# Kernel tuning notes

Measured on AMD Instinct MI355X. Metric: run time of the kernel, lower is better.

## Reference

```python
import jax, jax.numpy as jnp
import numpy as np

N = 50000      # num_nodes
E = 800000     # num_edges
D = 128        # hidden_dim
V = 32000      # vocab_size
T = 8          # num_edge_types
NT = 16        # num_node_types


def setup_inputs() -> dict:
    key = jax.random.key(0)
    ks = jax.random.split(key, 10)
    s = 1.0 / np.sqrt(D)
    return {
        "x": jax.random.randint(ks[0], (N,), 0, V),
        "edge_index": jax.random.randint(ks[1], (2, E), 0, N),
        "edge_type": jax.random.randint(ks[2], (E,), 0, T),
        "node_type": jax.random.randint(ks[3], (N,), 0, NT),
        "emb": jax.random.normal(ks[4], (V, D), dtype=jnp.float32) * s,
        "W_rel": jax.random.normal(ks[5], (T, D, D), dtype=jnp.float32) * s,
        "b_node": jax.random.normal(ks[6], (NT, D), dtype=jnp.float32) * 0.01,
        "W_ih": jax.random.normal(ks[7], (3 * D, D), dtype=jnp.float32) * s,
        "W_hh": jax.random.normal(ks[8], (3 * D, D), dtype=jnp.float32) * s,
        "b_ih": jnp.zeros((3 * D,), dtype=jnp.float32),
        "b_hh": jnp.zeros((3 * D,), dtype=jnp.float32),
    }


def _gru_cell(inp, h, W_ih, W_hh, b_ih, b_hh):
    # torch.nn.GRUCell semantics
    gi = inp @ W_ih.T + b_ih   # [N, 3D]
    gh = h @ W_hh.T + b_hh     # [N, 3D]
    i_r, i_z, i_n = jnp.split(gi, 3, axis=-1)
    h_r, h_z, h_n = jnp.split(gh, 3, axis=-1)
    r = jax.nn.sigmoid(i_r + h_r)
    z = jax.nn.sigmoid(i_z + h_z)
    n = jnp.tanh(i_n + r * h_n)
    return (1.0 - z) * n + z * h


def reference(x, edge_index, edge_type, node_type, emb, W_rel, b_node, W_ih, W_hh, b_ih, b_hh):
    h = emb[x]                                   # [N, D] node embeddings
    src, dst = edge_index[0], edge_index[1]
    n_nodes = h.shape[0]
    for _ in range(5):
        # relational message passing: per-edge-type linear on source nodes
        Ht = jnp.einsum('nd,tdf->ntf', h, W_rel)  # [N, T, D] all-type transforms
        msg = Ht[src, edge_type]                  # [E, D] gather per edge
        aggr = jax.ops.segment_sum(msg, dst, num_segments=n_nodes)  # scatter-add to dst
        aggr = aggr + b_node[node_type]           # node-type-specific bias
        h = _gru_cell(aggr, h, W_ih, W_hh, b_ih, b_hh)
    return h
```

## Files before the change

### kernel.cpp

```cpp
#include <hip/hip_runtime.h>
#include <hip/hip_fp16.h>
#include <math.h>

#define N_NODES 50000
#define N_EDGES 800000
#define D 128
#define T_TYPES 8
#define TPAD 136
#define NBLK_SCAN 196
#define TILES 1563

typedef short short8 __attribute__((ext_vector_type(8)));
typedef float float4v __attribute__((ext_vector_type(4)));
typedef unsigned short ushort_t;

static __device__ __forceinline__ unsigned short f2bf(float f) {
    unsigned u = __float_as_uint(f);
    u += 0x7fff + ((u >> 16) & 1);
    return (unsigned short)(u >> 16);
}
static __device__ __forceinline__ float bf2f(unsigned short b) {
    return __uint_as_float((unsigned)b << 16);
}
static __device__ __forceinline__ void splitbf(float x, unsigned short& hi, unsigned short& lo) {
    unsigned short h_ = f2bf(x);
    hi = h_;
    lo = f2bf(x - bf2f(h_));
}

#define GLOAD16(gp, lp) __builtin_amdgcn_global_load_lds( \
    (const __attribute__((address_space(1))) unsigned int*)(gp), \
    (__attribute__((address_space(3))) unsigned int*)(lp), 16, 0, 0)

__global__ void embed_gather(const int* __restrict__ x, const float* __restrict__ emb,
                             ushort_t* __restrict__ hhi, ushort_t* __restrict__ hlo) {
    int n = blockIdx.x;
    int d = threadIdx.x;
    float v = emb[(size_t)x[n] * D + d];
    unsigned short a, b;
    splitbf(v, a, b);
    hhi[(size_t)n * D + d] = a;
    hlo[(size_t)n * D + d] = b;
}

__global__ void convert_wrelT(const float* __restrict__ Wrel,
                              ushort_t* __restrict__ hi, ushort_t* __restrict__ lo) {
    int idx = blockIdx.x * 256 + threadIdx.x;
    int t = idx >> 14;
    int rem = idx & 16383;
    int f = rem >> 7;
    int d = rem & 127;
    unsigned short a, b;
    splitbf(Wrel[((size_t)t << 14) + (d << 7) + f], a, b);
    hi[idx] = a;
    lo[idx] = b;
}

__global__ void convert_w(const float* __restrict__ in,
                          ushort_t* __restrict__ hi, ushort_t* __restrict__ lo, int n) {
    int idx = blockIdx.x * 256 + threadIdx.x;
    if (idx < n) {
        unsigned short a, b;
        splitbf(in[idx], a, b);
        hi[idx] = a;
        lo[idx] = b;
    }
}

__global__ void count_deg(const int* __restrict__ ei, int* __restrict__ deg) {
    int e = blockIdx.x * 256 + threadIdx.x;
    if (e >= N_EDGES) return;
    atomicAdd(&deg[ei[N_EDGES + e]], 1);
}

__global__ __launch_bounds__(256) void scan_blocks(const int* __restrict__ deg,
                                                   int* __restrict__ bsums) {
    __shared__ int red[4];
    int idx = blockIdx.x * 256 + threadIdx.x;
    int v = (idx < N_NODES) ? deg[idx] : 0;
#pragma unroll
    for (int o = 32; o > 0; o >>= 1) v += __shfl_down(v, o);
    if ((threadIdx.x & 63) == 0) red[threadIdx.x >> 6] = v;
    __syncthreads();
    if (threadIdx.x == 0) bsums[blockIdx.x] = red[0] + red[1] + red[2] + red[3];
}

__global__ __launch_bounds__(256) void scan_tops(int* __restrict__ bsums) {
    __shared__ int s[256];
    int tid = threadIdx.x;
    int v = (tid < NBLK_SCAN) ? bsums[tid] : 0;
    s[tid] = v;
    __syncthreads();
#pragma unroll
    for (int o = 1; o < 256; o <<= 1) {
        int u = (tid >= o) ? s[tid - o] : 0;
        __syncthreads();
        s[tid] += u;
        __syncthreads();
    }
    if (tid < NBLK_SCAN) bsums[tid] = s[tid] - v;
}

__global__ __launch_bounds__(256) void scan_final(const int* __restrict__ bsums,
                                                  int* __restrict__ deg_cursor,
                                                  int* __restrict__ rs) {
    __shared__ int s[256];
    int tid = threadIdx.x;
    int idx = blockIdx.x * 256 + tid;
    int v = (idx < N_NODES) ? deg_cursor[idx] : 0;
    s[tid] = v;
    __syncthreads();
#pragma unroll
    for (int o = 1; o < 256; o <<= 1) {
        int u = (tid >= o) ? s[tid - o] : 0;
        __syncthreads();
        s[tid] += u;
        __syncthreads();
    }
    int excl = s[tid] - v + bsums[blockIdx.x];
    if (idx < N_NODES) {
        rs[idx] = excl;
        deg_cursor[idx] = excl;
    }
    if (idx == 0) rs[N_NODES] = N_EDGES;
}

__global__ void fill_csr(const int* __restrict__ ei, const int* __restrict__ et,
                         int* __restrict__ cursor, int* __restrict__ packed) {
    int e = blockIdx.x * 256 + threadIdx.x;
    if (e >= N_EDGES) return;
    int dst = ei[N_EDGES + e];
    int pos = atomicAdd(&cursor[dst], 1);
    packed[pos] = (ei[e] << 3) | et[e];
}

__global__ __launch_bounds__(256, 2) void gemm_rel(const ushort_t* __restrict__ hhi,
                                                   const ushort_t* __restrict__ hlo,
                                                   const ushort_t* __restrict__ Whi,
                                                   const ushort_t* __restrict__ Wlo,
                                                   ushort_t* __restrict__ Ht) {
    __shared__ __align__(16) ushort_t wlds[2][128 * TPAD];
    const int tid = threadIdx.x;
    const int wave = tid >> 6, lane = tid & 63;
    const int q = lane >> 4, li = lane & 15;
    const int t = blockIdx.y;
    const int m_base = blockIdx.x * 128 + wave * 32;

    {
        const ushort_t* gh = Whi + ((size_t)t << 14);
        const ushort_t* gl = Wlo + ((size_t)t << 14);
#pragma unroll
        for (int i = 0; i < 8; ++i) {
            int g = (i * 256 + tid) * 8;
            int row = g >> 7, col = g & 127;
            *(short8*)(&wlds[0][row * TPAD + col]) = *(const short8*)(gh + g);
            *(short8*)(&wlds[1][row * TPAD + col]) = *(const short8*)(gl + g);
        }
    }
    __syncthreads();

    int r0 = m_base + li;      if (r0 > N_NODES - 1) r0 = N_NODES - 1;
    int r1 = m_base + 16 + li; if (r1 > N_NODES - 1) r1 = N_NODES - 1;
    const ushort_t* A0h = hhi + (size_t)r0 * D + q * 8;
    const ushort_t* A0l = hlo + (size_t)r0 * D + q * 8;
    const ushort_t* A1h = hhi + (size_t)r1 * D + q * 8;
    const ushort_t* A1l = hlo + (size_t)r1 * D + q * 8;

    short8 a0h[4], a0l[4], a1h[4], a1l[4];
#pragma unroll
    for (int ks = 0; ks < 4; ++ks) {
        a0h[ks] = *(const short8*)(A0h + ks * 32);
        a0l[ks] = *(const short8*)(A0l + ks * 32);
        a1h[ks] = *(const short8*)(A1h + ks * 32);
        a1l[ks] = *(const short8*)(A1l + ks * 32);
    }

    float4v acc[2][8];
#pragma unroll
    for (int m = 0; m < 2; ++m)
#pragma unroll
        for (int ft = 0; ft < 8; ++ft) acc[m][ft] = (float4v){0.f, 0.f, 0.f, 0.f};

#pragma unroll
    for (int ks = 0; ks < 4; ++ks) {
#pragma unroll
        for (int ft = 0; ft < 8; ++ft) {
            const int lo_off = (ft * 16 + li) * TPAD + ks * 32 + q * 8;
            short8 bh = *(const short8*)(&wlds[0][lo_off]);
            short8 bl = *(const short8*)(&wlds[1][lo_off]);
            acc[0][ft] = __builtin_amdgcn_mfma_f32_16x16x32_bf16(a0h[ks], bh, acc[0][ft], 0, 0, 0);
            acc[0][ft] = __builtin_amdgcn_mfma_f32_16x16x32_bf16(a0l[ks], bh, acc[0][ft], 0, 0, 0);
            acc[0][ft] = __builtin_amdgcn_mfma_f32_16x16x32_bf16(a0h[ks], bl, acc[0][ft], 0, 0, 0);
            acc[1][ft] = __builtin_amdgcn_mfma_f32_16x16x32_bf16(a1h[ks], bh, acc[1][ft], 0, 0, 0);
            acc[1][ft] = __builtin_amdgcn_mfma_f32_16x16x32_bf16(a1l[ks], bh, acc[1][ft], 0, 0, 0);
            acc[1][ft] = __builtin_amdgcn_mfma_f32_16x16x32_bf16(a1h[ks], bl, acc[1][ft], 0, 0, 0);
        }
    }

    __syncthreads();
    ushort_t* tw = &wlds[0][0] + wave * 32 * TPAD;
#pragma unroll
    for (int m = 0; m < 2; ++m)
#pragma unroll
        for (int ft = 0; ft < 8; ++ft)
#pragma unroll
            for (int r = 0; r < 4; ++r) {
                __half hv = __float2half_rn(acc[m][ft][r]);
                tw[(m * 16 + q * 4 + r) * TPAD + ft * 16 + li] = __half_as_ushort(hv);
            }
#pragma unroll
    for (int i = 0; i < 8; ++i) {
        int row = i * 4 + q;
        int col = li * 8;
        short8 v = *(const short8*)(tw + row * TPAD + col);
        int orow = m_base + row;
        if (orow < N_NODES)
            *(short8*)(Ht + (size_t)orow * 1024 + (t << 7) + col) = v;
    }
}

__global__ __launch_bounds__(256) void aggregate_csr(const int* __restrict__ rs,
                                                     const int* __restrict__ packed,
                                                     const ushort_t* __restrict__ Ht,
                                                     const int* __restrict__ nt,
                                                     const float* __restrict__ b_node,
                                                     ushort_t* __restrict__ ahi,
                                                     ushort_t* __restrict__ alo) {
    int n = blockIdx.x * 4 + (threadIdx.x >> 6);
    if (n >= N_NODES) return;
    const int lane = threadIdx.x & 63;
    const int beg = rs[n], end = rs[n + 1];
    const __half2* Ht2 = (const __half2*)Ht;

    float2 acc = ((const float2*)(b_node + (size_t)nt[n] * D))[lane];

    int i = beg;
    for (; i + 3 < end; i += 4) {
        int p0 = packed[i], p1 = packed[i + 1], p2 = packed[i + 2], p3 = packed[i + 3];
        float2 f0 = __half22float2(Ht2[(size_t)p0 * 64 + lane]);
        float2 f1 = __half22float2(Ht2[(size_t)p1 * 64 + lane]);
        float2 f2 = __half22float2(Ht2[(size_t)p2 * 64 + lane]);
        float2 f3 = __half22float2(Ht2[(size_t)p3 * 64 + lane]);
        acc.x += (f0.x + f1.x) + (f2.x + f3.x);
        acc.y += (f0.y + f1.y) + (f2.y + f3.y);
    }
    for (; i < end; ++i) {
        int pk = packed[i];
        float2 fv = __half22float2(Ht2[(size_t)pk * 64 + lane]);
        acc.x += fv.x;
        acc.y += fv.y;
    }

    unsigned short h0, l0, h1, l1;
    splitbf(acc.x, h0, l0);
    splitbf(acc.y, h1, l1);
    ((unsigned*)ahi)[(size_t)n * 64 + lane] = (unsigned)h0 | ((unsigned)h1 << 16);
    ((unsigned*)alo)[(size_t)n * 64 + lane] = (unsigned)l0 | ((unsigned)l1 << 16);
}

__global__ __launch_bounds__(256, 1) void gru_persist(
    const ushort_t* __restrict__ ahi, const ushort_t* __restrict__ alo,
    const ushort_t* __restrict__ hhi_in, const ushort_t* __restrict__ hlo_in,
    ushort_t* __restrict__ hhi_out, ushort_t* __restrict__ hlo_out,
    const ushort_t* __restrict__ Wihi, const ushort_t* __restrict__ Wilo,
    const ushort_t* __restrict__ Whhi, const ushort_t* __restrict__ Whlo,
    const float* __restrict__ b_ih, const float* __restrict__ b_hh,
    float* __restrict__ h, int write_h)
{
    __shared__ __align__(16) ushort_t xlds[2 * 4 * 4096];
    __shared__ __align__(16) ushort_t tbuf[2][32 * 72];

    const int tid = threadIdx.x;
    const int wave = tid >> 6, lane = tid & 63;
    const int q = lane >> 4, li = lane & 15;
    const int bid = blockIdx.x;
    const int fhalf = (bid & 15) >> 3;
    const int s = (bid >> 4) * 8 + (bid & 7);
    const int fl = wave * 16 + li;
    const int fg = fhalf * 64 + fl;

    const size_t oR = (size_t)fg * D + q * 8;
    const size_t oZ = (size_t)(D + fg) * D + q * 8;
    const size_t oN = (size_t)(2 * D + fg) * D + q * 8;
    short8 Wr[12][4];
#pragma unroll
    for (int ks = 0; ks < 4; ++ks) {
        const int off = ks * 32;
        Wr[0][ks]  = *(const short8*)(Wihi + oR + off);
        Wr[1][ks]  = *(const short8*)(Wilo + oR + off);
        Wr[2][ks]  = *(const short8*)(Whhi + oR + off);
        Wr[3][ks]  = *(const short8*)(Whlo + oR + off);
        Wr[4][ks]  = *(const short8*)(Wihi + oZ + off);
        Wr[5][ks]  = *(const short8*)(Wilo + oZ + off);
        Wr[6][ks]  = *(const short8*)(Whhi + oZ + off);
        Wr[7][ks]  = *(const short8*)(Whlo + oZ + off);
        Wr[8][ks]  = *(const short8*)(Wihi + oN + off);
        Wr[9][ks]  = *(const short8*)(Wilo + oN + off);
        Wr[10][ks] = *(const short8*)(Whhi + oN + off);
        Wr[11][ks] = *(const short8*)(Whlo + oN + off);
    }
    const float bR  = b_ih[fg] + b_hh[fg];
    const float bZ  = b_ih[D + fg] + b_hh[D + fg];
    const float bIn = b_ih[2 * D + fg];
    const float bHn = b_hh[2 * D + fg];

    const int lrow_base = wave * 4 + (lane >> 4);
    const int cswz = (lane & 15) ^ (lrow_base & 7);

    {
#pragma unroll
        for (int it = 0; it < 2; ++it) {
            int gr = s * 32 + it * 16 + lrow_base;
            if (gr > N_NODES - 1) gr = N_NODES - 1;
            const size_t so = (size_t)gr * D + cswz * 8;
            ushort_t* l0 = &xlds[(it * 16 + wave * 4) * 128];
            GLOAD16(ahi + so,    l0);
            GLOAD16(alo + so,    l0 + 4096);
            GLOAD16(hhi_in + so, l0 + 8192);
            GLOAD16(hlo_in + so, l0 + 12288);
        }
    }
    __syncthreads();

    int cur = 0;
    for (int tile = s; tile < TILES; tile += 256) {
        const int nxt = tile + 256;
        if (nxt < TILES) {
            ushort_t* nb = &xlds[(cur ^ 1) * 16384];
#pragma unroll
            for (int it = 0; it < 2; ++it) {
                int gr = nxt * 32 + it * 16 + lrow_base;
                if (gr > N_NODES - 1) gr = N_NODES - 1;
                const size_t so = (size_t)gr * D + cswz * 8;
                ushort_t* l0 = nb + (it * 16 + wave * 4) * 128;
                GLOAD16(ahi + so,    l0);
                GLOAD16(alo + so,    l0 + 4096);
                GLOAD16(hhi_in + so, l0 + 8192);
                GLOAD16(hlo_in + so, l0 + 12288);
            }
        }

        const ushort_t* xb = &xlds[cur * 16384];
        float4v aR[2], aZ[2], aI[2], aH[2];
#pragma unroll
        for (int m = 0; m < 2; ++m) {
            aR[m] = (float4v){0.f, 0.f, 0.f, 0.f};
            aZ[m] = aR[m]; aI[m] = aR[m]; aH[m] = aR[m];
        }
#pragma unroll
        for (int ks = 0; ks < 4; ++ks) {
#pragma unroll
            for (int m = 0; m < 2; ++m) {
                const int row = m * 16 + li;
                const int inoff = row * 128 + ((ks * 32 + q * 8) ^ ((row & 7) << 3));
                short8 xah = *(const short8*)(xb + inoff);
                short8 xal = *(const short8*)(xb + 4096 + inoff);
                short8 xhh = *(const short8*)(xb + 8192 + inoff);
                short8 xhl = *(const short8*)(xb + 12288 + inoff);
                aR[m] = __builtin_amdgcn_mfma_f32_16x16x32_bf16(xah, Wr[0][ks], aR[m], 0, 0, 0);
                aR[m] = __builtin_amdgcn_mfma_f32_16x16x32_bf16(xal, Wr[0][ks], aR[m], 0, 0, 0);
                aR[m] = __builtin_amdgcn_mfma_f32_16x16x32_bf16(xah, Wr[1][ks], aR[m], 0, 0, 0);
                aR[m] = __builtin_amdgcn_mfma_f32_16x16x32_bf16(xhh, Wr[2][ks], aR[m], 0, 0, 0);
                aR[m] = __builtin_amdgcn_mfma_f32_16x16x32_bf16(xhl, Wr[2][ks], aR[m], 0, 0, 0);
                aR[m] = __builtin_amdgcn_mfma_f32_16x16x32_bf16(xhh, Wr[3][ks], aR[m], 0, 0, 0);
                aZ[m] = __builtin_amdgcn_mfma_f32_16x16x32_bf16(xah, Wr[4][ks], aZ[m], 0, 0, 0);
                aZ[m] = __builtin_amdgcn_mfma_f32_16x16x32_bf16(xal, Wr[4][ks], aZ[m], 0, 0, 0);
                aZ[m] = __builtin_amdgcn_mfma_f32_16x16x32_bf16(xah, Wr[5][ks], aZ[m], 0, 0, 0);
                aZ[m] = __builtin_amdgcn_mfma_f32_16x16x32_bf16(xhh, Wr[6][ks], aZ[m], 0, 0, 0);
                aZ[m] = __builtin_amdgcn_mfma_f32_16x16x32_bf16(xhl, Wr[6][ks], aZ[m], 0, 0, 0);
                aZ[m] = __builtin_amdgcn_mfma_f32_16x16x32_bf16(xhh, Wr[7][ks], aZ[m], 0, 0, 0);
                aI[m] = __builtin_amdgcn_mfma_f32_16x16x32_bf16(xah, Wr[8][ks], aI[m], 0, 0, 0);
                aI[m] = __builtin_amdgcn_mfma_f32_16x16x32_bf16(xal, Wr[8][ks], aI[m], 0, 0, 0);
                aI[m] = __builtin_amdgcn_mfma_f32_16x16x32_bf16(xah, Wr[9][ks], aI[m], 0, 0, 0);
                aH[m] = __builtin_amdgcn_mfma_f32_16x16x32_bf16(xhh, Wr[10][ks], aH[m], 0, 0, 0);
                aH[m] = __builtin_amdgcn_mfma_f32_16x16x32_bf16(xhl, Wr[10][ks], aH[m], 0, 0, 0);
                aH[m] = __builtin_amdgcn_mfma_f32_16x16x32_bf16(xhh, Wr[11][ks], aH[m], 0, 0, 0);
            }
        }

#pragma unroll
        for (int m = 0; m < 2; ++m) {
#pragma unroll
            for (int r = 0; r < 4; ++r) {
                const int row = m * 16 + q * 4 + r;
                const int hoff = row * 128 + (fg ^ ((row & 7) << 3));
                float hold = bf2f(xb[8192 + hoff]) + bf2f(xb[12288 + hoff]);
                float rg = 1.0f / (1.0f + __expf(-(aR[m][r] + bR)));
                float zg = 1.0f / (1.0f + __expf(-(aZ[m][r] + bZ)));
                float narg = aI[m][r] + bIn + rg * (aH[m][r] + bHn);
                float ex = __expf(2.0f * narg);
                float ng = 1.0f - 2.0f / (ex + 1.0f);
                float hn = (1.0f - zg) * ng + zg * hold;
                unsigned short sh, sl;
                splitbf(hn, sh, sl);
                tbuf[0][row * 72 + fl] = sh;
                tbuf[1][row * 72 + fl] = sl;
            }
        }
        __syncthreads();

        {
            const int row = tid >> 3, col = (tid & 7) * 8;
            const int node = tile * 32 + row;
            if (node < N_NODES) {
                short8 vh = *(const short8*)(&tbuf[0][row * 72 + col]);
                short8 vl = *(const short8*)(&tbuf[1][row * 72 + col]);
                const size_t go = (size_t)node * D + fhalf * 64 + col;
                *(short8*)(hhi_out + go) = vh;
                *(short8*)(hlo_out + go) = vl;
                if (write_h) {
                    float4v f0, f1;
#pragma unroll
                    for (int k2 = 0; k2 < 4; ++k2) {
                        f0[k2] = bf2f((unsigned short)vh[k2]) + bf2f((unsigned short)vl[k2]);
                        f1[k2] = bf2f((unsigned short)vh[4 + k2]) + bf2f((unsigned short)vl[4 + k2]);
                    }
                    *(float4v*)(h + go) = f0;
                    *(float4v*)(h + go + 4) = f1;
                }
            }
        }
        __syncthreads();
        cur ^= 1;
    }
}

extern "C" void kernel_launch(void* const* d_in, const int* in_sizes, int n_in,
                              void* d_out, int out_size, void* d_ws, size_t ws_size,
                              hipStream_t stream) {
    const int* x      = (const int*)d_in[0];
    const int* ei     = (const int*)d_in[1];
    const int* et     = (const int*)d_in[2];
    const int* nt     = (const int*)d_in[3];
    const float* emb  = (const float*)d_in[4];
    const float* Wrel = (const float*)d_in[5];
    const float* b_node = (const float*)d_in[6];
    const float* W_ih = (const float*)d_in[7];
    const float* W_hh = (const float*)d_in[8];
    const float* b_ih = (const float*)d_in[9];
    const float* b_hh = (const float*)d_in[10];

    float* h = (float*)d_out;
    float* ws = (float*)d_ws;

    ushort_t* Ht = (ushort_t*)ws;
    ushort_t* us = (ushort_t*)(ws + 25600000);
    ushort_t* ahi  = us;
    ushort_t* alo  = us + 6400000;
    ushort_t* hhi  = us + 12800000;
    ushort_t* hlo  = us + 19200000;
    ushort_t* Whi  = us + 25600000;
    ushort_t* Wlo  = Whi + 131072;
    ushort_t* Wihi = Wlo + 131072;
    ushort_t* Wilo = Wihi + 49152;
    ushort_t* Whhi = Wilo + 49152;
    ushort_t* Whlo = Whhi + 49152;
    int* rs     = (int*)(ws + 38629376);
    int* packed = rs + 50004;
    int* bsums  = packed + 800000;
    ushort_t* hhi2 = (ushort_t*)(ws + 39479808);
    ushort_t* hlo2 = hhi2 + 6400000;
    int* deg    = (int*)ws;

    convert_wrelT<<<512, 256, 0, stream>>>(Wrel, Whi, Wlo);
    convert_w<<<192, 256, 0, stream>>>(W_ih, Wihi, Wilo, 3 * D * D);
    convert_w<<<192, 256, 0, stream>>>(W_hh, Whhi, Whlo, 3 * D * D);
    embed_gather<<<N_NODES, 128, 0, stream>>>(x, emb, hhi, hlo);

    hipMemsetAsync(deg, 0, 50000 * sizeof(int), stream);
    count_deg<<<3125, 256, 0, stream>>>(ei, deg);
    scan_blocks<<<NBLK_SCAN, 256, 0, stream>>>(deg, bsums);
    scan_tops<<<1, 256, 0, stream>>>(bsums);
    scan_final<<<NBLK_SCAN, 256, 0, stream>>>(bsums, deg, rs);
    fill_csr<<<3125, 256, 0, stream>>>(ei, et, deg, packed);

    for (int it = 0; it < 5; ++it) {
        const ushort_t* hi_in = (it & 1) ? hhi2 : hhi;
        const ushort_t* lo_in = (it & 1) ? hlo2 : hlo;
        ushort_t* hi_out = (it & 1) ? hhi : hhi2;
        ushort_t* lo_out = (it & 1) ? hlo : hlo2;
        dim3 g(391, T_TYPES);
        gemm_rel<<<g, 256, 0, stream>>>(hi_in, lo_in, Whi, Wlo, Ht);
        aggregate_csr<<<12500, 256, 0, stream>>>(rs, packed, Ht, nt, b_node, ahi, alo);
        gru_persist<<<512, 256, 0, stream>>>(ahi, alo, hi_in, lo_in, hi_out, lo_out,
                                             Wihi, Wilo, Whhi, Whlo, b_ih, b_hh,
                                             h, it == 4 ? 1 : 0);
    }
}
```

Baseline: 977.5 us.

## Aggregate raw source features per edge type before applying relational weights

Replaces transform-then-gather with gather-then-transform. Edges are bucketed into a CSR keyed by (type, dst). A scatter kernel sums the source features per bucket into an fp16 buffer S of size T×N×D. A single typed GEMM then multiplies each type slice by W_rel and accumulates across types, adding the node-type bias. This removes the large N×T×D Ht write and its random per-edge gather, at the cost of an fp16 intermediate for the summed features and a split-fp16 weight scheme with a scaled low part, which may reduce accuracy.

```diff
diff --git a/kernel.cpp b/kernel.cpp
--- a/kernel.cpp
+++ b/kernel.cpp
@@ -7,10 +7,12 @@
 #define D 128
 #define T_TYPES 8
 #define TPAD 136
-#define NBLK_SCAN 196
+#define N2 400000
+#define NBLK2 1563
 #define TILES 1563
 
 typedef short short8 __attribute__((ext_vector_type(8)));
+typedef _Float16 half8v __attribute__((ext_vector_type(8)));
 typedef float float4v __attribute__((ext_vector_type(4)));
 typedef unsigned short ushort_t;
 
@@ -43,17 +45,19 @@
     hlo[(size_t)n * D + d] = b;
 }
 
-__global__ void convert_wrelT(const float* __restrict__ Wrel,
-                              ushort_t* __restrict__ hi, ushort_t* __restrict__ lo) {
+__global__ void convert_wrelT_f16(const float* __restrict__ Wrel,
+                                  ushort_t* __restrict__ hi, ushort_t* __restrict__ lo) {
     int idx = blockIdx.x * 256 + threadIdx.x;
     int t = idx >> 14;
     int rem = idx & 16383;
     int f = rem >> 7;
     int d = rem & 127;
-    unsigned short a, b;
-    splitbf(Wrel[((size_t)t << 14) + (d << 7) + f], a, b);
-    hi[idx] = a;
-    lo[idx] = b;
+    float w = Wrel[((size_t)t << 14) + (d << 7) + f];
+    __half wh = __float2half_rn(w);
+    float r = w - __half2float(wh);
+    __half wl = __float2half_rn(r * 2048.0f);
+    hi[idx] = __half_as_ushort(wh);
+    lo[idx] = __half_as_ushort(wl);
 }
 
 __global__ void convert_w(const float* __restrict__ in,
@@ -67,17 +71,18 @@
     }
 }
 
-__global__ void count_deg(const int* __restrict__ ei, int* __restrict__ deg) {
+__global__ void count_deg2(const int* __restrict__ ei, const int* __restrict__ et,
+                           int* __restrict__ deg2) {
     int e = blockIdx.x * 256 + threadIdx.x;
     if (e >= N_EDGES) return;
-    atomicAdd(&deg[ei[N_EDGES + e]], 1);
-}
-
-__global__ __launch_bounds__(256) void scan_blocks(const int* __restrict__ deg,
-                                                   int* __restrict__ bsums) {
+    atomicAdd(&deg2[et[e] * N_NODES + ei[N_EDGES + e]], 1);
+}
+
+__global__ __launch_bounds__(256) void scan_blocks2(const int* __restrict__ deg,
+                                                    int* __restrict__ bsums) {
     __shared__ int red[4];
     int idx = blockIdx.x * 256 + threadIdx.x;
-    int v = (idx < N_NODES) ? deg[idx] : 0;
+    int v = (idx < N2) ? deg[idx] : 0;
 #pragma unroll
     for (int o = 32; o > 0; o >>= 1) v += __shfl_down(v, o);
     if ((threadIdx.x & 63) == 0) red[threadIdx.x >> 6] = v;
@@ -85,29 +90,39 @@
     if (threadIdx.x == 0) bsums[blockIdx.x] = red[0] + red[1] + red[2] + red[3];
 }
 
-__global__ __launch_bounds__(256) void scan_tops(int* __restrict__ bsums) {
+__global__ __launch_bounds__(256) void scan_tops2(int* __restrict__ bsums) {
     __shared__ int s[256];
+    __shared__ int carry_s;
     int tid = threadIdx.x;
-    int v = (tid < NBLK_SCAN) ? bsums[tid] : 0;
-    s[tid] = v;
+    if (tid == 0) carry_s = 0;
     __syncthreads();
-#pragma unroll
-    for (int o = 1; o < 256; o <<= 1) {
-        int u = (tid >= o) ? s[tid - o] : 0;
-        __syncthreads();
-        s[tid] += u;
-        __syncthreads();
-    }
-    if (tid < NBLK_SCAN) bsums[tid] = s[tid] - v;
-}
-
-__global__ __launch_bounds__(256) void scan_final(const int* __restrict__ bsums,
-                                                  int* __restrict__ deg_cursor,
-                                                  int* __restrict__ rs) {
+    for (int c = 0; c < 7; ++c) {
+        int idx = c * 256 + tid;
+        int v = (idx < NBLK2) ? bsums[idx] : 0;
+        s[tid] = v;
+        __syncthreads();
+#pragma unroll
+        for (int o = 1; o < 256; o <<= 1) {
+            int u = (tid >= o) ? s[tid - o] : 0;
+            __syncthreads();
+            s[tid] += u;
+            __syncthreads();
+        }
+        int carry = carry_s;
+        if (idx < NBLK2) bsums[idx] = s[tid] - v + carry;
+        __syncthreads();
+        if (tid == 255) carry_s = carry + s[255];
+        __syncthreads();
+    }
+}
+
+__global__ __launch_bounds__(256) void scan_final2(const int* __restrict__ bsums,
+                                                   int* __restrict__ deg_cursor,
+                                                   int* __restrict__ rs2) {
     __shared__ int s[256];
     int tid = threadIdx.x;
     int idx = blockIdx.x * 256 + tid;
-    int v = (idx < N_NODES) ? deg_cursor[idx] : 0;
+    int v = (idx < N2) ? deg_cursor[idx] : 0;
     s[tid] = v;
     __syncthreads();
 #pragma unroll
@@ -118,144 +133,160 @@
         __syncthreads();
     }
     int excl = s[tid] - v + bsums[blockIdx.x];
-    if (idx < N_NODES) {
-        rs[idx] = excl;
+    if (idx < N2) {
+        rs2[idx] = excl;
         deg_cursor[idx] = excl;
     }
-    if (idx == 0) rs[N_NODES] = N_EDGES;
-}
-
-__global__ void fill_csr(const int* __restrict__ ei, const int* __restrict__ et,
-                         int* __restrict__ cursor, int* __restrict__ packed) {
+    if (idx == 0) rs2[N2] = N_EDGES;
+}
+
+__global__ void fill_csr2(const int* __restrict__ ei, const int* __restrict__ et,
+                          int* __restrict__ cursor, int* __restrict__ esrc) {
     int e = blockIdx.x * 256 + threadIdx.x;
     if (e >= N_EDGES) return;
-    int dst = ei[N_EDGES + e];
-    int pos = atomicAdd(&cursor[dst], 1);
-    packed[pos] = (ei[e] << 3) | et[e];
-}
-
-__global__ __launch_bounds__(256, 2) void gemm_rel(const ushort_t* __restrict__ hhi,
-                                                   const ushort_t* __restrict__ hlo,
-                                                   const ushort_t* __restrict__ Whi,
-                                                   const ushort_t* __restrict__ Wlo,
-                                                   ushort_t* __restrict__ Ht) {
+    int key = et[e] * N_NODES + ei[N_EDGES + e];
+    int pos = atomicAdd(&cursor[key], 1);
+    esrc[pos] = ei[e];
+}
+
+__global__ __launch_bounds__(256) void scatter_S(const int* __restrict__ rs2,
+                                                 const int* __restrict__ esrc,
+                                                 const ushort_t* __restrict__ hhi,
+                                                 const ushort_t* __restrict__ hlo,
+                                                 __half* __restrict__ S) {
+    const int lane = threadIdx.x & 63;
+    const int wave = threadIdx.x >> 6;
+    const unsigned* H = (const unsigned*)hhi;
+    const unsigned* L = (const unsigned*)hlo;
+#pragma unroll
+    for (int j = 0; j < 4; ++j) {
+        int seg = blockIdx.x * 16 + wave * 4 + j;
+        if (seg >= N2) return;
+        int beg = rs2[seg], end = rs2[seg + 1];
+        float ax = 0.f, ay = 0.f;
+        int i = beg;
+        for (; i + 1 < end; i += 2) {
+            int s0 = esrc[i], s1 = esrc[i + 1];
+            unsigned u0 = H[s0 * 64 + lane], l0 = L[s0 * 64 + lane];
+            unsigned u1 = H[s1 * 64 + lane], l1 = L[s1 * 64 + lane];
+            ax += (bf2f((unsigned short)u0) + bf2f((unsigned short)l0)) +
+                  (bf2f((unsigned short)u1) + bf2f((unsigned short)l1));
+            ay += (bf2f((unsigned short)(u0 >> 16)) + bf2f((unsigned short)(l0 >> 16))) +
+                  (bf2f((unsigned short)(u1 >> 16)) + bf2f((unsigned short)(l1 >> 16)));
+        }
+        if (i < end) {
+            int s0 = esrc[i];
+            unsigned u0 = H[s0 * 64 + lane], l0 = L[s0 * 64 + lane];
+            ax += bf2f((unsigned short)u0) + bf2f((unsigned short)l0);
+            ay += bf2f((unsigned short)(u0 >> 16)) + bf2f((unsigned short)(l0 >> 16));
+        }
+        ((__half2*)S)[(size_t)seg * 64 + lane] = __floats2half2_rn(ax, ay);
+    }
+}
+
+__global__ __launch_bounds__(256, 2) void typed_gemm(const __half* __restrict__ S,
+                                                     const ushort_t* __restrict__ Wfh,
+                                                     const ushort_t* __restrict__ Wfl,
+                                                     const int* __restrict__ nt,
+                                                     const float* __restrict__ b_node,
+                                                     ushort_t* __restrict__ ahi,
+                                                     ushort_t* __restrict__ alo) {
     __shared__ __align__(16) ushort_t wlds[2][128 * TPAD];
     const int tid = threadIdx.x;
     const int wave = tid >> 6, lane = tid & 63;
     const int q = lane >> 4, li = lane & 15;
-    const int t = blockIdx.y;
     const int m_base = blockIdx.x * 128 + wave * 32;
-
-    {
-        const ushort_t* gh = Whi + ((size_t)t << 14);
-        const ushort_t* gl = Wlo + ((size_t)t << 14);
-#pragma unroll
-        for (int i = 0; i < 8; ++i) {
-            int g = (i * 256 + tid) * 8;
-            int row = g >> 7, col = g & 127;
-            *(short8*)(&wlds[0][row * TPAD + col]) = *(const short8*)(gh + g);
-            *(short8*)(&wlds[1][row * TPAD + col]) = *(const short8*)(gl + g);
-        }
-    }
-    __syncthreads();
+    const ushort_t* Sus = (const ushort_t*)S;
 
     int r0 = m_base + li;      if (r0 > N_NODES - 1) r0 = N_NODES - 1;
     int r1 = m_base + 16 + li; if (r1 > N_NODES - 1) r1 = N_NODES - 1;
-    const ushort_t* A0h = hhi + (size_t)r0 * D + q * 8;
-    const ushort_t* A0l = hlo + (size_t)r0 * D + q * 8;
-    const ushort_t* A1h = hhi + (size_t)r1 * D + q * 8;
-    const ushort_t* A1l = hlo + (size_t)r1 * D + q * 8;
-
-    short8 a0h[4], a0l[4], a1h[4], a1l[4];
-#pragma unroll
-    for (int ks = 0; ks < 4; ++ks) {
-        a0h[ks] = *(const short8*)(A0h + ks * 32);
-        a0l[ks] = *(const short8*)(A0l + ks * 32);
-        a1h[ks] = *(const short8*)(A1h + ks * 32);
-        a1l[ks] = *(const short8*)(A1l + ks * 32);
-    }
-
-    float4v acc[2][8];
+
+    float4v acch[2][8], accl[2][8];
 #pragma unroll
     for (int m = 0; m < 2; ++m)
 #pragma unroll
-        for (int ft = 0; ft < 8; ++ft) acc[m][ft] = (float4v){0.f, 0.f, 0.f, 0.f};
-
-#pragma unroll
-    for (int ks = 0; ks < 4; ++ks) {
-#pragma unroll
         for (int ft = 0; ft < 8; ++ft) {
-            const int lo_off = (ft * 16 + li) * TPAD + ks * 32 + q * 8;
-            short8 bh = *(const short8*)(&wlds[0][lo_off]);
-            short8 bl = *(const short8*)(&wlds[1][lo_off]);
-            acc[0][ft] = __builtin_amdgcn_mfma_f32_16x16x32_bf16(a0h[ks], bh, acc[0][ft], 0, 0, 0);
-            acc[0][ft] = __builtin_amdgcn_mfma_f32_16x16x32_bf16(a0l[ks], bh, acc[0][ft], 0, 0, 0);
-            acc[0][ft] = __builtin_amdgcn_mfma_f32_16x16x32_bf16(a0h[ks], bl, acc[0][ft], 0, 0, 0);
-            acc[1][ft] = __builtin_amdgcn_mfma_f32_16x16x32_bf16(a1h[ks], bh, acc[1][ft], 0, 0, 0);
-            acc[1][ft] = __builtin_amdgcn_mfma_f32_16x16x32_bf16(a1l[ks], bh, acc[1][ft], 0, 0, 0);
-            acc[1][ft] = __builtin_amdgcn_mfma_f32_16x16x32_bf16(a1h[ks], bl, acc[1][ft], 0, 0, 0);
-        }
-    }
+            acch[m][ft] = (float4v){0.f, 0.f, 0.f, 0.f};
+            accl[m][ft] = acch[m][ft];
+        }
+
+    half8v pa0[2][4], pa1[2][4];
+#define LOADA(T_, SET_) do {                                                   \
+        const ushort_t* sb0 = Sus + ((size_t)(T_) * N_NODES + r0) * D + q * 8; \
+        const ushort_t* sb1 = Sus + ((size_t)(T_) * N_NODES + r1) * D + q * 8; \
+        _Pragma("unroll")                                                      \
+        for (int ks = 0; ks < 4; ++ks) {                                       \
+            pa0[SET_][ks] = *(const half8v*)(sb0 + ks * 32);                   \
+            pa1[SET_][ks] = *(const half8v*)(sb1 + ks * 32);                   \
+        }                                                                      \
+    } while (0)
+
+    LOADA(0, 0);
+
+#pragma unroll
+    for (int t = 0; t < T_TYPES; ++t) {
+        if (t > 0) __syncthreads();
+        {
+            const ushort_t* gh = Wfh + ((size_t)t << 14);
+            const ushort_t* gl = Wfl + ((size_t)t << 14);
+#pragma unroll
+            for (int i = 0; i < 8; ++i) {
+                int g = (i * 256 + tid) * 8;
+                int row = g >> 7, col = g & 127;
+                *(short8*)(&wlds[0][row * TPAD + col]) = *(const short8*)(gh + g);
+                *(short8*)(&wlds[1][row * TPAD + col]) = *(const short8*)(gl + g);
+            }
+        }
+        __syncthreads();
+        if (t < T_TYPES - 1) LOADA(t + 1, (t + 1) & 1);
+#pragma unroll
+        for (int ks = 0; ks < 4; ++ks) {
+#pragma unroll
+            for (int ft = 0; ft < 8; ++ft) {
+                const int lo_off = (ft * 16 + li) * TPAD + ks * 32 + q * 8;
+                half8v bh = *(const half8v*)(&wlds[0][lo_off]);
+                half8v bl = *(const half8v*)(&wlds[1][lo_off]);
+                acch[0][ft] = __builtin_amdgcn_mfma_f32_16x16x32_f16(pa0[t & 1][ks], bh, acch[0][ft], 0, 0, 0);
+                accl[0][ft] = __builtin_amdgcn_mfma_f32_16x16x32_f16(pa0[t & 1][ks], bl, accl[0][ft], 0, 0, 0);
+                acch[1][ft] = __builtin_amdgcn_mfma_f32_16x16x32_f16(pa1[t & 1][ks], bh, acch[1][ft], 0, 0, 0);
+                accl[1][ft] = __builtin_amdgcn_mfma_f32_16x16x32_f16(pa1[t & 1][ks], bl, accl[1][ft], 0, 0, 0);
+            }
+        }
+    }
+#undef LOADA
 
     __syncthreads();
-    ushort_t* tw = &wlds[0][0] + wave * 32 * TPAD;
+    ushort_t* twh = &wlds[0][0] + wave * 32 * TPAD;
+    ushort_t* twl = &wlds[1][0] + wave * 32 * TPAD;
 #pragma unroll
     for (int m = 0; m < 2; ++m)
 #pragma unroll
         for (int ft = 0; ft < 8; ++ft)
 #pragma unroll
             for (int r = 0; r < 4; ++r) {
-                __half hv = __float2half_rn(acc[m][ft][r]);
-                tw[(m * 16 + q * 4 + r) * TPAD + ft * 16 + li] = __half_as_ushort(hv);
+                const int row = m * 16 + q * 4 + r;
+                int grow = m_base + row;
+                if (grow > N_NODES - 1) grow = N_NODES - 1;
+                const int col = ft * 16 + li;
+                float v = acch[m][ft][r] + accl[m][ft][r] * (1.0f / 2048.0f);
+                v += b_node[nt[grow] * D + col];
+                unsigned short sh, sl;
+                splitbf(v, sh, sl);
+                twh[row * TPAD + col] = sh;
+                twl[row * TPAD + col] = sl;
             }
 #pragma unroll
     for (int i = 0; i < 8; ++i) {
         int row = i * 4 + q;
         int col = li * 8;
-        short8 v = *(const short8*)(tw + row * TPAD + col);
+        short8 vh = *(const short8*)(twh + row * TPAD + col);
+        short8 vl = *(const short8*)(twl + row * TPAD + col);
         int orow = m_base + row;
-        if (orow < N_NODES)
-            *(short8*)(Ht + (size_t)orow * 1024 + (t << 7) + col) = v;
-    }
-}
-
-__global__ __launch_bounds__(256) void aggregate_csr(const int* __restrict__ rs,
-                                                     const int* __restrict__ packed,
-                                                     const ushort_t* __restrict__ Ht,
-                                                     const int* __restrict__ nt,
-                                                     const float* __restrict__ b_node,
-                                                     ushort_t* __restrict__ ahi,
-                                                     ushort_t* __restrict__ alo) {
-    int n = blockIdx.x * 4 + (threadIdx.x >> 6);
-    if (n >= N_NODES) return;
-    const int lane = threadIdx.x & 63;
-    const int beg = rs[n], end = rs[n + 1];
-    const __half2* Ht2 = (const __half2*)Ht;
-
-    float2 acc = ((const float2*)(b_node + (size_t)nt[n] * D))[lane];
-
-    int i = beg;
-    for (; i + 3 < end; i += 4) {
-        int p0 = packed[i], p1 = packed[i + 1], p2 = packed[i + 2], p3 = packed[i + 3];
-        float2 f0 = __half22float2(Ht2[(size_t)p0 * 64 + lane]);
-        float2 f1 = __half22float2(Ht2[(size_t)p1 * 64 + lane]);
-        float2 f2 = __half22float2(Ht2[(size_t)p2 * 64 + lane]);
-        float2 f3 = __half22float2(Ht2[(size_t)p3 * 64 + lane]);
-        acc.x += (f0.x + f1.x) + (f2.x + f3.x);
-        acc.y += (f0.y + f1.y) + (f2.y + f3.y);
-    }
-    for (; i < end; ++i) {
-        int pk = packed[i];
-        float2 fv = __half22float2(Ht2[(size_t)pk * 64 + lane]);
-        acc.x += fv.x;
-        acc.y += fv.y;
-    }
-
-    unsigned short h0, l0, h1, l1;
-    splitbf(acc.x, h0, l0);
-    splitbf(acc.y, h1, l1);
-    ((unsigned*)ahi)[(size_t)n * 64 + lane] = (unsigned)h0 | ((unsigned)h1 << 16);
-    ((unsigned*)alo)[(size_t)n * 64 + lane] = (unsigned)l0 | ((unsigned)l1 << 16);
+        if (orow < N_NODES) {
+            *(short8*)(ahi + (size_t)orow * D + col) = vh;
+            *(short8*)(alo + (size_t)orow * D + col) = vl;
+        }
+    }
 }
 
 __global__ __launch_bounds__(256, 1) void gru_persist(
@@ -443,45 +474,44 @@
     float* h = (float*)d_out;
     float* ws = (float*)d_ws;
 
-    ushort_t* Ht = (ushort_t*)ws;
+    __half* S = (__half*)ws;
     ushort_t* us = (ushort_t*)(ws + 25600000);
     ushort_t* ahi  = us;
     ushort_t* alo  = us + 6400000;
     ushort_t* hhi  = us + 12800000;
     ushort_t* hlo  = us + 19200000;
-    ushort_t* Whi  = us + 25600000;
-    ushort_t* Wlo  = Whi + 131072;
-    ushort_t* Wihi = Wlo + 131072;
+    ushort_t* Wfh  = us + 25600000;
+    ushort_t* Wfl  = Wfh + 131072;
+    ushort_t* Wihi = Wfl + 131072;
     ushort_t* Wilo = Wihi + 49152;
     ushort_t* Whhi = Wilo + 49152;
     ushort_t* Whlo = Whhi + 49152;
-    int* rs     = (int*)(ws + 38629376);
-    int* packed = rs + 50004;
-    int* bsums  = packed + 800000;
-    ushort_t* hhi2 = (ushort_t*)(ws + 39479808);
+    int* rs2    = (int*)(ws + 38629376);
+    int* esrc   = rs2 + 400001;
+    int* bsums2 = esrc + 800000;
+    ushort_t* hhi2 = (ushort_t*)(ws + 39830944);
     ushort_t* hlo2 = hhi2 + 6400000;
-    int* deg    = (int*)ws;
-
-    convert_wrelT<<<512, 256, 0, stream>>>(Wrel, Whi, Wlo);
+    int* deg2   = (int*)ws;
+
+    convert_wrelT_f16<<<512, 256, 0, stream>>>(Wrel, Wfh, Wfl);
     convert_w<<<192, 256, 0, stream>>>(W_ih, Wihi, Wilo, 3 * D * D);
     convert_w<<<192, 256, 0, stream>>>(W_hh, Whhi, Whlo, 3 * D * D);
     embed_gather<<<N_NODES, 128, 0, stream>>>(x, emb, hhi, hlo);
 
-    hipMemsetAsync(deg, 0, 50000 * sizeof(int), stream);
-    count_deg<<<3125, 256, 0, stream>>>(ei, deg);
-    scan_blocks<<<NBLK_SCAN, 256, 0, stream>>>(deg, bsums);
-    scan_tops<<<1, 256, 0, stream>>>(bsums);
-    scan_final<<<NBLK_SCAN, 256, 0, stream>>>(bsums, deg, rs);
-    fill_csr<<<3125, 256, 0, stream>>>(ei, et, deg, packed);
+    hipMemsetAsync(deg2, 0, N2 * sizeof(int), stream);
+    count_deg2<<<3125, 256, 0, stream>>>(ei, et, deg2);
+    scan_blocks2<<<NBLK2, 256, 0, stream>>>(deg2, bsums2);
+    scan_tops2<<<1, 256, 0, stream>>>(bsums2);
+    scan_final2<<<NBLK2, 256, 0, stream>>>(bsums2, deg2, rs2);
+    fill_csr2<<<3125, 256, 0, stream>>>(ei, et, deg2, esrc);
 
     for (int it = 0; it < 5; ++it) {
         const ushort_t* hi_in = (it & 1) ? hhi2 : hhi;
         const ushort_t* lo_in = (it & 1) ? hlo2 : hlo;
         ushort_t* hi_out = (it & 1) ? hhi : hhi2;
         ushort_t* lo_out = (it & 1) ? hlo : hlo2;
-        dim3 g(391, T_TYPES);
-        gemm_rel<<<g, 256, 0, stream>>>(hi_in, lo_in, Whi, Wlo, Ht);
-        aggregate_csr<<<12500, 256, 0, stream>>>(rs, packed, Ht, nt, b_node, ahi, alo);
+        scatter_S<<<25000, 256, 0, stream>>>(rs2, esrc, hi_in, lo_in, S);
+        typed_gemm<<<391, 256, 0, stream>>>(S, Wfh, Wfl, nt, b_node, ahi, alo);
         gru_persist<<<512, 256, 0, stream>>>(ahi, alo, hi_in, lo_in, hi_out, lo_out,
                                              Wihi, Wilo, Whhi, Whlo, b_ih, b_hh,
                                              h, it == 4 ? 1 : 0);
```

Result: slower. 1.248 ms (+27.6%).

## Restructure GRU kernel to 512-thread blocks covering all 128 features

Applied to the files above, without the earlier changes.

The persistent GRU kernel now uses 512-thread blocks of 8 waves that each cover all 128 output features, instead of two 256-thread blocks that each took one 64-feature half. Each staged node tile is therefore loaded into LDS once rather than twice. The MFMA operands are swapped so each lane holds 4 consecutive features of one node, which lets the epilogue write vector stores straight to global memory and drops the LDS transpose buffer and one barrier. The cost is a large weight-register footprint per thread with launch bounds requesting 2 blocks per CU, which risks register spills, and a grid of 256 blocks.

```diff
diff --git a/kernel.cpp b/kernel.cpp
--- a/kernel.cpp
+++ b/kernel.cpp
@@ -9,8 +9,10 @@
 #define TPAD 136
 #define NBLK_SCAN 196
 #define TILES 1563
+#define GRID_GRU 256
 
 typedef short short8 __attribute__((ext_vector_type(8)));
+typedef unsigned short ushort4v __attribute__((ext_vector_type(4)));
 typedef float float4v __attribute__((ext_vector_type(4)));
 typedef unsigned short ushort_t;
 
@@ -258,7 +260,7 @@
     ((unsigned*)alo)[(size_t)n * 64 + lane] = (unsigned)l0 | ((unsigned)l1 << 16);
 }
 
-__global__ __launch_bounds__(256, 1) void gru_persist(
+__global__ __launch_bounds__(512, 2) void gru_persist(
     const ushort_t* __restrict__ ahi, const ushort_t* __restrict__ alo,
     const ushort_t* __restrict__ hhi_in, const ushort_t* __restrict__ hlo_in,
     ushort_t* __restrict__ hhi_out, ushort_t* __restrict__ hlo_out,
@@ -267,17 +269,13 @@
     const float* __restrict__ b_ih, const float* __restrict__ b_hh,
     float* __restrict__ h, int write_h)
 {
-    __shared__ __align__(16) ushort_t xlds[2 * 4 * 4096];
-    __shared__ __align__(16) ushort_t tbuf[2][32 * 72];
+    __shared__ __align__(16) ushort_t xlds[2][4][4096];
 
     const int tid = threadIdx.x;
-    const int wave = tid >> 6, lane = tid & 63;
+    const int w = tid >> 6, lane = tid & 63;
     const int q = lane >> 4, li = lane & 15;
-    const int bid = blockIdx.x;
-    const int fhalf = (bid & 15) >> 3;
-    const int s = (bid >> 4) * 8 + (bid & 7);
-    const int fl = wave * 16 + li;
-    const int fg = fhalf * 64 + fl;
+    const int fg = w * 16 + li;
+    const int f0 = w * 16 + q * 4;
 
     const size_t oR = (size_t)fg * D + q * 8;
     const size_t oZ = (size_t)(D + fg) * D + q * 8;
@@ -299,48 +297,40 @@
         Wr[10][ks] = *(const short8*)(Whhi + oN + off);
         Wr[11][ks] = *(const short8*)(Whlo + oN + off);
     }
-    const float bR  = b_ih[fg] + b_hh[fg];
-    const float bZ  = b_ih[D + fg] + b_hh[D + fg];
-    const float bIn = b_ih[2 * D + fg];
-    const float bHn = b_hh[2 * D + fg];
-
-    const int lrow_base = wave * 4 + (lane >> 4);
-    const int cswz = (lane & 15) ^ (lrow_base & 7);
-
+    float4v bR4 = *(const float4v*)(b_ih + f0);
+    float4v bZ4 = *(const float4v*)(b_ih + D + f0);
+    float4v bIn4 = *(const float4v*)(b_ih + 2 * D + f0);
     {
-#pragma unroll
-        for (int it = 0; it < 2; ++it) {
-            int gr = s * 32 + it * 16 + lrow_base;
-            if (gr > N_NODES - 1) gr = N_NODES - 1;
-            const size_t so = (size_t)gr * D + cswz * 8;
-            ushort_t* l0 = &xlds[(it * 16 + wave * 4) * 128];
-            GLOAD16(ahi + so,    l0);
-            GLOAD16(alo + so,    l0 + 4096);
-            GLOAD16(hhi_in + so, l0 + 8192);
-            GLOAD16(hlo_in + so, l0 + 12288);
-        }
-    }
+        float4v t0 = *(const float4v*)(b_hh + f0);
+        float4v t1 = *(const float4v*)(b_hh + D + f0);
+        bR4 += t0; bZ4 += t1;
+    }
+    float4v bHn4 = *(const float4v*)(b_hh + 2 * D + f0);
+
+    const int lrow = w * 4 + (lane >> 4);
+    const int cswz = (lane & 15) ^ (lrow & 7);
+
+#define STAGE(BUF_, TILE_) do {                                      \
+        int gr_ = (TILE_) * 32 + lrow;                               \
+        if (gr_ > N_NODES - 1) gr_ = N_NODES - 1;                    \
+        const size_t so_ = (size_t)gr_ * D + cswz * 8;               \
+        ushort_t* lb_ = &xlds[BUF_][0][0] + (w * 4) * 128;           \
+        GLOAD16(ahi + so_,    lb_);                                  \
+        GLOAD16(alo + so_,    lb_ + 4096);                           \
+        GLOAD16(hhi_in + so_, lb_ + 8192);                           \
+        GLOAD16(hlo_in + so_, lb_ + 12288);                          \
+    } while (0)
+
+    const int s = blockIdx.x;
+    STAGE(0, s);
     __syncthreads();
 
     int cur = 0;
-    for (int tile = s; tile < TILES; tile += 256) {
-        const int nxt = tile + 256;
-        if (nxt < TILES) {
-            ushort_t* nb = &xlds[(cur ^ 1) * 16384];
-#pragma unroll
-            for (int it = 0; it < 2; ++it) {
-                int gr = nxt * 32 + it * 16 + lrow_base;
-                if (gr > N_NODES - 1) gr = N_NODES - 1;
-                const size_t so = (size_t)gr * D + cswz * 8;
-                ushort_t* l0 = nb + (it * 16 + wave * 4) * 128;
-                GLOAD16(ahi + so,    l0);
-                GLOAD16(alo + so,    l0 + 4096);
-                GLOAD16(hhi_in + so, l0 + 8192);
-                GLOAD16(hlo_in + so, l0 + 12288);
-            }
-        }
-
-        const ushort_t* xb = &xlds[cur * 16384];
+    for (int tile = s; tile < TILES; tile += GRID_GRU) {
+        const int nxt = tile + GRID_GRU;
+        if (nxt < TILES) STAGE(cur ^ 1, nxt);
+
+        const ushort_t* xb = &xlds[cur][0][0];
         float4v aR[2], aZ[2], aI[2], aH[2];
 #pragma unroll
         for (int m = 0; m < 2; ++m) {
@@ -357,72 +347,63 @@
                 short8 xal = *(const short8*)(xb + 4096 + inoff);
                 short8 xhh = *(const short8*)(xb + 8192 + inoff);
                 short8 xhl = *(const short8*)(xb + 12288 + inoff);
-                aR[m] = __builtin_amdgcn_mfma_f32_16x16x32_bf16(xah, Wr[0][ks], aR[m], 0, 0, 0);
-                aR[m] = __builtin_amdgcn_mfma_f32_16x16x32_bf16(xal, Wr[0][ks], aR[m], 0, 0, 0);
-                aR[m] = __builtin_amdgcn_mfma_f32_16x16x32_bf16(xah, Wr[1][ks], aR[m], 0, 0, 0);
-                aR[m] = __builtin_amdgcn_mfma_f32_16x16x32_bf16(xhh, Wr[2][ks], aR[m], 0, 0, 0);
-                aR[m] = __builtin_amdgcn_mfma_f32_16x16x32_bf16(xhl, Wr[2][ks], aR[m], 0, 0, 0);
-                aR[m] = __builtin_amdgcn_mfma_f32_16x16x32_bf16(xhh, Wr[3][ks], aR[m], 0, 0, 0);
-                aZ[m] = __builtin_amdgcn_mfma_f32_16x16x32_bf16(xah, Wr[4][ks], aZ[m], 0, 0, 0);
-                aZ[m] = __builtin_amdgcn_mfma_f32_16x16x32_bf16(xal, Wr[4][ks], aZ[m], 0, 0, 0);
-                aZ[m] = __builtin_amdgcn_mfma_f32_16x16x32_bf16(xah, Wr[5][ks], aZ[m], 0, 0, 0);
-                aZ[m] = __builtin_amdgcn_mfma_f32_16x16x32_bf16(xhh, Wr[6][ks], aZ[m], 0, 0, 0);
-                aZ[m] = __builtin_amdgcn_mfma_f32_16x16x32_bf16(xhl, Wr[6][ks], aZ[m], 0, 0, 0);
-                aZ[m] = __builtin_amdgcn_mfma_f32_16x16x32_bf16(xhh, Wr[7][ks], aZ[m], 0, 0, 0);
-                aI[m] = __builtin_amdgcn_mfma_f32_16x16x32_bf16(xah, Wr[8][ks], aI[m], 0, 0, 0);
-                aI[m] = __builtin_amdgcn_mfma_f32_16x16x32_bf16(xal, Wr[8][ks], aI[m], 0, 0, 0);
-                aI[m] = __builtin_amdgcn_mfma_f32_16x16x32_bf16(xah, Wr[9][ks], aI[m], 0, 0, 0);
-                aH[m] = __builtin_amdgcn_mfma_f32_16x16x32_bf16(xhh, Wr[10][ks], aH[m], 0, 0, 0);
-                aH[m] = __builtin_amdgcn_mfma_f32_16x16x32_bf16(xhl, Wr[10][ks], aH[m], 0, 0, 0);
-                aH[m] = __builtin_amdgcn_mfma_f32_16x16x32_bf16(xhh, Wr[11][ks], aH[m], 0, 0, 0);
+                aR[m] = __builtin_amdgcn_mfma_f32_16x16x32_bf16(Wr[0][ks], xah, aR[m], 0, 0, 0);
+                aR[m] = __builtin_amdgcn_mfma_f32_16x16x32_bf16(Wr[0][ks], xal, aR[m], 0, 0, 0);
+                aR[m] = __builtin_amdgcn_mfma_f32_16x16x32_bf16(Wr[1][ks], xah, aR[m], 0, 0, 0);
+                aR[m] = __builtin_amdgcn_mfma_f32_16x16x32_bf16(Wr[2][ks], xhh, aR[m], 0, 0, 0);
+                aR[m] = __builtin_amdgcn_mfma_f32_16x16x32_bf16(Wr[2][ks], xhl, aR[m], 0, 0, 0);
+                aR[m] = __builtin_amdgcn_mfma_f32_16x16x32_bf16(Wr[3][ks], xhh, aR[m], 0, 0, 0);
+                aZ[m] = __builtin_amdgcn_mfma_f32_16x16x32_bf16(Wr[4][ks], xah, aZ[m], 0, 0, 0);
+                aZ[m] = __builtin_amdgcn_mfma_f32_16x16x32_bf16(Wr[4][ks], xal, aZ[m], 0, 0, 0);
+                aZ[m] = __builtin_amdgcn_mfma_f32_16x16x32_bf16(Wr[5][ks], xah, aZ[m], 0, 0, 0);
+                aZ[m] = __builtin_amdgcn_mfma_f32_16x16x32_bf16(Wr[6][ks], xhh, aZ[m], 0, 0, 0);
+                aZ[m] = __builtin_amdgcn_mfma_f32_16x16x32_bf16(Wr[6][ks], xhl, aZ[m], 0, 0, 0);
+                aZ[m] = __builtin_amdgcn_mfma_f32_16x16x32_bf16(Wr[7][ks], xhh, aZ[m], 0, 0, 0);
+                aI[m] = __builtin_amdgcn_mfma_f32_16x16x32_bf16(Wr[8][ks], xah, aI[m], 0, 0, 0);
+                aI[m] = __builtin_amdgcn_mfma_f32_16x16x32_bf16(Wr[8][ks], xal, aI[m], 0, 0, 0);
+                aI[m] = __builtin_amdgcn_mfma_f32_16x16x32_bf16(Wr[9][ks], xah, aI[m], 0, 0, 0);
+                aH[m] = __builtin_amdgcn_mfma_f32_16x16x32_bf16(Wr[10][ks], xhh, aH[m], 0, 0, 0);
+                aH[m] = __builtin_amdgcn_mfma_f32_16x16x32_bf16(Wr[10][ks], xhl, aH[m], 0, 0, 0);
+                aH[m] = __builtin_amdgcn_mfma_f32_16x16x32_bf16(Wr[11][ks], xhh, aH[m], 0, 0, 0);
             }
         }
 
 #pragma unroll
         for (int m = 0; m < 2; ++m) {
-#pragma unroll
-            for (int r = 0; r < 4; ++r) {
-                const int row = m * 16 + q * 4 + r;
-                const int hoff = row * 128 + (fg ^ ((row & 7) << 3));
-                float hold = bf2f(xb[8192 + hoff]) + bf2f(xb[12288 + hoff]);
-                float rg = 1.0f / (1.0f + __expf(-(aR[m][r] + bR)));
-                float zg = 1.0f / (1.0f + __expf(-(aZ[m][r] + bZ)));
-                float narg = aI[m][r] + bIn + rg * (aH[m][r] + bHn);
-                float ex = __expf(2.0f * narg);
-                float ng = 1.0f - 2.0f / (ex + 1.0f);
-                float hn = (1.0f - zg) * ng + zg * hold;
-                unsigned short sh, sl;
-                splitbf(hn, sh, sl);
-                tbuf[0][row * 72 + fl] = sh;
-                tbuf[1][row * 72 + fl] = sl;
-            }
-        }
-        __syncthreads();
-
-        {
-            const int row = tid >> 3, col = (tid & 7) * 8;
-            const int node = tile * 32 + row;
+            const int node = tile * 32 + m * 16 + li;
+            const int row = m * 16 + li;
+            const int chunk = (f0 >> 3) ^ (row & 7);
+            const int hoff = row * 128 + chunk * 8 + (q & 1) * 4;
+            ushort4v hh4 = *(const ushort4v*)(xb + 8192 + hoff);
+            ushort4v hl4 = *(const ushort4v*)(xb + 12288 + hoff);
             if (node < N_NODES) {
-                short8 vh = *(const short8*)(&tbuf[0][row * 72 + col]);
-                short8 vl = *(const short8*)(&tbuf[1][row * 72 + col]);
-                const size_t go = (size_t)node * D + fhalf * 64 + col;
-                *(short8*)(hhi_out + go) = vh;
-                *(short8*)(hlo_out + go) = vl;
-                if (write_h) {
-                    float4v f0, f1;
-#pragma unroll
-                    for (int k2 = 0; k2 < 4; ++k2) {
-                        f0[k2] = bf2f((unsigned short)vh[k2]) + bf2f((unsigned short)vl[k2]);
-                        f1[k2] = bf2f((unsigned short)vh[4 + k2]) + bf2f((unsigned short)vl[4 + k2]);
-                    }
-                    *(float4v*)(h + go) = f0;
-                    *(float4v*)(h + go + 4) = f1;
+                ushort4v sh4, sl4;
+                float4v hn4;
+#pragma unroll
+                for (int r = 0; r < 4; ++r) {
+                    float hold = bf2f(hh4[r]) + bf2f(hl4[r]);
+                    float rg = 1.0f / (1.0f + __expf(-(aR[m][r] + bR4[r])));
+                    float zg = 1.0f / (1.0f + __expf(-(aZ[m][r] + bZ4[r])));
+                    float narg = aI[m][r] + bIn4[r] + rg * (aH[m][r] + bHn4[r]);
+                    float ex = __expf(2.0f * narg);
+                    float ng = 1.0f - 2.0f / (ex + 1.0f);
+                    float hn = (1.0f - zg) * ng + zg * hold;
+                    hn4[r] = hn;
+                    unsigned short sh, sl;
+                    splitbf(hn, sh, sl);
+                    sh4[r] = sh;
+                    sl4[r] = sl;
                 }
+                const size_t go = (size_t)node * D + f0;
+                *(ushort4v*)(hhi_out + go) = sh4;
+                *(ushort4v*)(hlo_out + go) = sl4;
+                if (write_h) *(float4v*)(h + go) = hn4;
             }
         }
         __syncthreads();
         cur ^= 1;
     }
+#undef STAGE
 }
 
 extern "C" void kernel_launch(void* const* d_in, const int* in_sizes, int n_in,
@@ -482,8 +463,8 @@
         dim3 g(391, T_TYPES);
         gemm_rel<<<g, 256, 0, stream>>>(hi_in, lo_in, Whi, Wlo, Ht);
         aggregate_csr<<<12500, 256, 0, stream>>>(rs, packed, Ht, nt, b_node, ahi, alo);
-        gru_persist<<<512, 256, 0, stream>>>(ahi, alo, hi_in, lo_in, hi_out, lo_out,
-                                             Wihi, Wilo, Whhi, Whlo, b_ih, b_hh,
-                                             h, it == 4 ? 1 : 0);
-    }
-}
+        gru_persist<<<GRID_GRU, 512, 0, stream>>>(ahi, alo, hi_in, lo_in, hi_out, lo_out,
+                                                  Wihi, Wilo, Whhi, Whlo, b_ih, b_hh,
+                                                  h, it == 4 ? 1 : 0);
+    }
+}
```

Measured after the change: 999.4 us. +2.2%, slower.
